# Kernel optimization log

Hardware: AMD Instinct MI355X
Metric: run time of the kernel (lower is better)

## Reference

```python
import jax, jax.numpy as jnp
import numpy as np
from jax import lax

BS, T, D, H, FF, KS, L = 8, 1024, 512, 8, 2048, 5, 6
DK = D // H  # 64


def setup_inputs() -> dict:
    key = jax.random.key(0)
    ks_ = jax.random.split(key, 16)
    n = lambda i, shape, s=0.02: jax.random.normal(ks_[i], shape, jnp.float32) * s
    return dict(
        q_embed_data=n(0, (BS, T, D), 1.0),
        qa_embed_data=n(1, (BS, T, D), 1.0),
        pid_embed_data=n(2, (BS, T, T), 1.0),  # unused for emb_type='qid'
        conv_w=n(3, (D, D, KS)), conv_b=jnp.zeros((D,), jnp.float32),
        sqrt_beta=n(4, (1, 1, D), 1.0),
        sm_g=jnp.ones((D,), jnp.float32), sm_b=jnp.zeros((D,), jnp.float32),
        k_w=n(5, (L, D, D)), k_b=jnp.zeros((L, D), jnp.float32),
        v_w=n(6, (L, D, D)), v_b=jnp.zeros((L, D), jnp.float32),
        out_w=n(7, (L, D, D)), out_b=jnp.zeros((L, D), jnp.float32),
        gammas=n(8, (L, H, 1, 1), 0.1),
        ln1_g=jnp.ones((L, D), jnp.float32), ln1_b=jnp.zeros((L, D), jnp.float32),
        ff1_w=n(9, (L, D, FF)), ff1_b=jnp.zeros((L, FF), jnp.float32),
        ff2_w=n(10, (L, FF, D)), ff2_b=jnp.zeros((L, D), jnp.float32),
        ln2_g=jnp.ones((L, D), jnp.float32), ln2_b=jnp.zeros((L, D), jnp.float32),
    )


def _layernorm(x, g, b, eps):
    m = jnp.mean(x, axis=-1, keepdims=True)
    v = jnp.mean((x - m) ** 2, axis=-1, keepdims=True)
    return g * (x - m) / jnp.sqrt(v + eps) + b


def _smooth(x, conv_w, conv_b, sqrt_beta, g, b):
    # x: [B,T,D]. Causal Conv1d: left-pad KS-1, crop to length T.
    xt = jnp.transpose(x, (0, 2, 1))  # [B,D,T]
    trend = lax.conv_general_dilated(
        xt, conv_w, window_strides=(1,), padding=[(KS - 1, 0)],
        dimension_numbers=('NCH', 'OIH', 'NCH')) + conv_b[None, :, None]
    trend = jnp.transpose(trend, (0, 2, 1))  # [B,T,D]
    random = x - trend
    seq = trend + sqrt_beta ** 2 * random
    return _layernorm(seq + x, g, b, 1e-12)


def _decay_attention(q, k, v, mask, gamma_param, zero_pad):
    # q,k,v: [B,H,T,DK]; mask: [1,1,T,T] bool
    neg = jnp.float32(-1e32)
    scores = jnp.einsum('bhqd,bhkd->bhqk', q, k) / np.float32(np.sqrt(DK))
    # detached distance-effect computation (no_grad in torch)
    s_ = jax.nn.softmax(jnp.where(mask, scores, neg), axis=-1) * mask.astype(jnp.float32)
    distcum = jnp.cumsum(s_, axis=-1)
    disttot = jnp.sum(s_, axis=-1, keepdims=True)
    idx = jnp.arange(T, dtype=jnp.float32)
    pos = jnp.abs(idx[None, :] - idx[:, None])[None, None]  # |j - i|
    dist = jnp.sqrt(jnp.clip((disttot - distcum) * pos, 0.0, None))
    dist = lax.stop_gradient(dist)
    gamma = -jax.nn.softplus(gamma_param)[None]  # [1,H,1,1]
    total_effect = jnp.clip(jnp.exp(dist * gamma), 1e-5, 1e5)
    scores = jnp.where(mask, scores * total_effect, neg)
    scores = jax.nn.softmax(scores, axis=-1)
    if zero_pad:
        scores = scores.at[:, :, 0, :].set(0.0)
    return jnp.einsum('bhqk,bhkd->bhqd', scores, v)


def _tlayer(p, i, mtype, q_in, k_in, v_in, apply_pos, masks):
    mask = masks[mtype]
    def heads(x, W, b):
        return jnp.transpose((x @ W + b).reshape(BS, T, H, DK), (0, 2, 1, 3))
    # kq_same=True: q and k both use k_linear
    q = heads(q_in, p['k_w'][i], p['k_b'][i])
    k = heads(k_in, p['k_w'][i], p['k_b'][i])
    v = heads(v_in, p['v_w'][i], p['v_b'][i])
    out = _decay_attention(q, k, v, mask, p['gammas'][i], zero_pad=(mtype == 0))
    concat = jnp.transpose(out, (0, 2, 1, 3)).reshape(BS, T, D)
    q2 = concat @ p['out_w'][i] + p['out_b'][i]
    x = _layernorm(q_in + q2, p['ln1_g'][i], p['ln1_b'][i], 1e-5)
    if apply_pos:
        hdn = jax.nn.relu(x @ p['ff1_w'][i] + p['ff1_b'][i])
        x = _layernorm(x + hdn @ p['ff2_w'][i] + p['ff2_b'][i],
                       p['ln2_g'][i], p['ln2_b'][i], 1e-5)
    return x


def _forward(q_embed_data, qa_embed_data, pid_embed_data,
             conv_w, conv_b, sqrt_beta, sm_g, sm_b,
             k_w, k_b, v_w, v_b, out_w, out_b, gammas,
             ln1_g, ln1_b, ff1_w, ff1_b, ff2_w, ff2_b, ln2_g, ln2_b):
    p = dict(k_w=k_w, k_b=k_b, v_w=v_w, v_b=v_b, out_w=out_w, out_b=out_b,
             gammas=gammas, ln1_g=ln1_g, ln1_b=ln1_b, ff1_w=ff1_w, ff1_b=ff1_b,
             ff2_w=ff2_w, ff2_b=ff2_b, ln2_g=ln2_g, ln2_b=ln2_b)
    tri = jnp.tril(jnp.ones((T, T), bool))
    masks = {1: tri[None, None], 0: jnp.tril(jnp.ones((T, T), bool), -1)[None, None]}
    x = _smooth(q_embed_data, conv_w, conv_b, sqrt_beta, sm_g, sm_b)
    y = _smooth(qa_embed_data, conv_w, conv_b, sqrt_beta, sm_g, sm_b)
    # blocks_1: n_blocks=2 layers, mask=1, self-attn on y
    y = _tlayer(p, 0, 1, y, y, y, True, masks)
    y = _tlayer(p, 1, 1, y, y, y, True, masks)
    # blocks_2: 4 layers alternating (mask=1, no FFN) / (mask=0, values=y, FFN)
    x = _tlayer(p, 2, 1, x, x, x, False, masks)
    x = _tlayer(p, 3, 0, x, x, y, True, masks)
    x = _tlayer(p, 4, 1, x, x, x, False, masks)
    x = _tlayer(p, 5, 0, x, x, y, True, masks)
    return x


def reference(q_embed_data, qa_embed_data, pid_embed_data,
              conv_w, conv_b, sqrt_beta, sm_g, sm_b,
              k_w, k_b, v_w, v_b, out_w, out_b, gammas,
              ln1_g, ln1_b, ff1_w, ff1_b, ff2_w, ff2_b, ln2_g, ln2_b):
    return _forward(q_embed_data, qa_embed_data, pid_embed_data,
                    conv_w, conv_b, sqrt_beta, sm_g, sm_b,
                    k_w, k_b, v_w, v_b, out_w, out_b, gammas,
                    ln1_g, ln1_b, ff1_w, ff1_b, ff2_w, ff2_b, ln2_g, ln2_b)
```

## Files before the change

### kernel.cpp

```cpp
#include <hip/hip_runtime.h>
#include <math.h>

#define T_  1024
#define D_  512
#define H_  8
#define DK_ 64
#define FF_ 2048
#define BSZ 8
#define M_  (BSZ * T_)
#define TP_ (T_ + 4)

typedef unsigned short u16;
typedef unsigned int u32;
typedef __attribute__((ext_vector_type(8))) __bf16 bf16x8;
typedef __attribute__((ext_vector_type(4))) float f32x4;

__device__ __forceinline__ u16 f2bf(float f) {
    unsigned int u = __float_as_uint(f);
    u += 0x7fffu + ((u >> 16) & 1u);
    return (u16)(u >> 16);
}
__device__ __forceinline__ float bf2f(u16 b) {
    return __uint_as_float((unsigned int)b << 16);
}

__device__ __forceinline__ void gload16(const void* g, void* l) {
    __builtin_amdgcn_global_load_lds(
        (const __attribute__((address_space(1))) void*)g,
        (__attribute__((address_space(3))) void*)l, 16, 0, 0);
}

__global__ void __launch_bounds__(256) gemm_mfma(
    const u16* __restrict__ A, const u16* __restrict__ Bt,
    const float* __restrict__ bias, void* __restrict__ Cout,
    int N, int K, int mode)
{
    __shared__ __align__(16) u16 As[128 * 32];
    __shared__ __align__(16) u16 Bs[128 * 32];
    int tid = threadIdx.x;
    int wid = tid >> 6, lane = tid & 63;
    int quad = lane >> 4, mrow = lane & 15;
    int m0 = blockIdx.y * 128, n0 = blockIdx.x * 128;
    int wr = (wid >> 1) * 64, wc = (wid & 1) * 64;

    const u16* Ap = A + (size_t)(m0 + (tid >> 2)) * K + (tid & 3) * 8;
    const u16* Bp = Bt + (size_t)(n0 + (tid >> 2)) * K + (tid & 3) * 8;
    char* lA = (char*)As + wid * 1024;
    char* lB = (char*)Bs + wid * 1024;

    f32x4 acc[4][4] = {};
    for (int k0 = 0; k0 < K; k0 += 32) {
        __syncthreads();
        gload16(Ap + k0, lA);
        gload16(Ap + (size_t)64 * K + k0, lA + 4096);
        gload16(Bp + k0, lB);
        gload16(Bp + (size_t)64 * K + k0, lB + 4096);
        asm volatile("s_waitcnt vmcnt(0)" ::: "memory");
        __syncthreads();
        bf16x8 af[4], bf[4];
#pragma unroll
        for (int t = 0; t < 4; ++t) {
            af[t] = *(const bf16x8*)&As[(wr + t * 16 + mrow) * 32 + quad * 8];
            bf[t] = *(const bf16x8*)&Bs[(wc + t * 16 + mrow) * 32 + quad * 8];
        }
#pragma unroll
        for (int rt = 0; rt < 4; ++rt)
#pragma unroll
            for (int ct = 0; ct < 4; ++ct)
                acc[rt][ct] = __builtin_amdgcn_mfma_f32_16x16x32_bf16(
                    af[rt], bf[ct], acc[rt][ct], 0, 0, 0);
    }

#pragma unroll
    for (int ct = 0; ct < 4; ++ct) {
        int col = n0 + wc + ct * 16 + mrow;
        float bv = bias ? bias[col] : 0.f;
#pragma unroll
        for (int rt = 0; rt < 4; ++rt) {
            int rowb = m0 + wr + rt * 16 + quad * 4;
            if (mode == 0) {
                float* C = (float*)Cout;
#pragma unroll
                for (int e = 0; e < 4; ++e)
                    C[(size_t)(rowb + e) * N + col] = acc[rt][ct][e] + bv;
            } else if (mode == 1) {
                u16* C = (u16*)Cout;
#pragma unroll
                for (int e = 0; e < 4; ++e)
                    C[(size_t)(rowb + e) * N + col] = f2bf(fmaxf(acc[rt][ct][e] + bv, 0.f));
            } else {
                u16* C = (u16*)Cout;
#pragma unroll
                for (int e = 0; e < 4; ++e)
                    C[(size_t)(rowb + e) * N + col] = f2bf(acc[rt][ct][e] + bv);
            }
        }
    }
}

__global__ void __launch_bounds__(256) gemm64_mfma(
    const u16* __restrict__ A, const u16* __restrict__ Bt,
    const float* __restrict__ bias, void* __restrict__ Cout,
    int N, int K, int mode)
{
    __shared__ __align__(16) u16 As[2 * 64 * 32];
    __shared__ __align__(16) u16 Bs[2 * 64 * 32];
    int tid = threadIdx.x;
    int wid = tid >> 6, lane = tid & 63;
    int quad = lane >> 4, mrow = lane & 15;
    int m0 = blockIdx.y * 64, n0 = blockIdx.x * 64;
    int wc = wid * 16;

    const u16* Ap = A + (size_t)(m0 + (tid >> 2)) * K + (tid & 3) * 8;
    const u16* Bp = Bt + (size_t)(n0 + (tid >> 2)) * K + (tid & 3) * 8;
    char* lA = (char*)As + wid * 1024;
    char* lB = (char*)Bs + wid * 1024;

    f32x4 acc[4] = {};
    for (int k0 = 0; k0 < K; k0 += 64) {
        __syncthreads();
        gload16(Ap + k0, lA);
        gload16(Ap + k0 + 32, lA + 4096);
        gload16(Bp + k0, lB);
        gload16(Bp + k0 + 32, lB + 4096);
        asm volatile("s_waitcnt vmcnt(0)" ::: "memory");
        __syncthreads();
#pragma unroll
        for (int q = 0; q < 2; ++q) {
            bf16x8 af[4];
#pragma unroll
            for (int t = 0; t < 4; ++t)
                af[t] = *(const bf16x8*)&As[q * 2048 + (t * 16 + mrow) * 32 + quad * 8];
            bf16x8 bf = *(const bf16x8*)&Bs[q * 2048 + (wc + mrow) * 32 + quad * 8];
#pragma unroll
            for (int rt = 0; rt < 4; ++rt)
                acc[rt] = __builtin_amdgcn_mfma_f32_16x16x32_bf16(af[rt], bf, acc[rt], 0, 0, 0);
        }
    }

    int col = n0 + wc + mrow;
    float bv = bias ? bias[col] : 0.f;
#pragma unroll
    for (int rt = 0; rt < 4; ++rt) {
        int rowb = m0 + rt * 16 + quad * 4;
        if (mode == 0) {
            float* C = (float*)Cout;
#pragma unroll
            for (int e = 0; e < 4; ++e)
                C[(size_t)(rowb + e) * N + col] = acc[rt][e] + bv;
        } else if (mode == 1) {
            u16* C = (u16*)Cout;
#pragma unroll
            for (int e = 0; e < 4; ++e)
                C[(size_t)(rowb + e) * N + col] = f2bf(fmaxf(acc[rt][e] + bv, 0.f));
        } else if (mode == 2) {
            u16* C = (u16*)Cout;
#pragma unroll
            for (int e = 0; e < 4; ++e)
                C[(size_t)(rowb + e) * N + col] = f2bf(acc[rt][e] + bv);
        } else {
            u16* C = (u16*)Cout;
            int h = col >> 6, dl = col & 63;
#pragma unroll
            for (int e = 0; e < 4; ++e) {
                int row = rowb + e;
                int b = row >> 10, t = row & (T_ - 1);
                C[(((size_t)(b * H_ + h) * DK_ + dl) << 10) + t] =
                    f2bf(acc[rt][e] + bv);
            }
        }
    }
}

__global__ void __launch_bounds__(256) conv64_mfma(
    const u16* __restrict__ Xp, const u16* __restrict__ W5t, float* __restrict__ C)
{
    __shared__ __align__(16) u16 As[2 * 64 * 32];
    __shared__ __align__(16) u16 Bs[2 * 64 * 32];
    int tid = threadIdx.x;
    int wid = tid >> 6, lane = tid & 63;
    int quad = lane >> 4, mrow = lane & 15;
    int m0 = blockIdx.y * 64, n0 = blockIdx.x * 64;
    int wc = wid * 16;
    int b = m0 >> 10, tloc = m0 & (T_ - 1);

    const u16* Ap0 = Xp + (size_t)(b * TP_ + tloc + (tid >> 2)) * D_ + (tid & 3) * 8;
    const u16* Bp0 = W5t + (size_t)(n0 + (tid >> 2)) * D_ + (tid & 3) * 8;
    char* lA = (char*)As + wid * 1024;
    char* lB = (char*)Bs + wid * 1024;

    f32x4 acc[4] = {};
    for (int s = 0; s < 40; ++s) {
        int ks = s >> 3, k0 = (s & 7) * 64;
        const u16* Ap = Ap0 + ks * D_ + k0;
        const u16* Bp = Bp0 + (size_t)ks * D_ * D_ + k0;
        __syncthreads();
        gload16(Ap, lA);
        gload16(Ap + 32, lA + 4096);
        gload16(Bp, lB);
        gload16(Bp + 32, lB + 4096);
        asm volatile("s_waitcnt vmcnt(0)" ::: "memory");
        __syncthreads();
#pragma unroll
        for (int q = 0; q < 2; ++q) {
            bf16x8 af[4];
#pragma unroll
            for (int t = 0; t < 4; ++t)
                af[t] = *(const bf16x8*)&As[q * 2048 + (t * 16 + mrow) * 32 + quad * 8];
            bf16x8 bf = *(const bf16x8*)&Bs[q * 2048 + (wc + mrow) * 32 + quad * 8];
#pragma unroll
            for (int rt = 0; rt < 4; ++rt)
                acc[rt] = __builtin_amdgcn_mfma_f32_16x16x32_bf16(af[rt], bf, acc[rt], 0, 0, 0);
        }
    }
    int col = n0 + wc + mrow;
#pragma unroll
    for (int rt = 0; rt < 4; ++rt) {
        int row = m0 + rt * 16 + quad * 4;
#pragma unroll
        for (int e = 0; e < 4; ++e)
            C[(size_t)(row + e) * D_ + col] = acc[rt][e];
    }
}

__global__ void __launch_bounds__(256) qk_mfma(
    const u16* __restrict__ Qh, u16* __restrict__ S)
{
    int kt = blockIdx.x, it = blockIdx.y;
    if (kt > it) return;
    int z = blockIdx.z;
    int b = z >> 3, h = z & 7;
    __shared__ __align__(16) u16 As[2 * 64 * 32];
    __shared__ __align__(16) u16 Bs[2 * 64 * 32];
    int tid = threadIdx.x;
    int wid = tid >> 6, lane = tid & 63;
    int quad = lane >> 4, mrow = lane & 15;
    int wc = wid * 16;

    const u16* Ap = Qh + (size_t)(b * T_ + it * 64 + (tid >> 2)) * D_ + h * DK_ + (tid & 3) * 8;
    const u16* Bp = Qh + (size_t)(b * T_ + kt * 64 + (tid >> 2)) * D_ + h * DK_ + (tid & 3) * 8;
    char* lA = (char*)As + wid * 1024;
    char* lB = (char*)Bs + wid * 1024;

    gload16(Ap, lA);
    gload16(Ap + 32, lA + 4096);
    gload16(Bp, lB);
    gload16(Bp + 32, lB + 4096);
    asm volatile("s_waitcnt vmcnt(0)" ::: "memory");
    __syncthreads();

    f32x4 acc[4] = {};
#pragma unroll
    for (int q = 0; q < 2; ++q) {
        bf16x8 af[4];
#pragma unroll
        for (int t = 0; t < 4; ++t)
            af[t] = *(const bf16x8*)&As[q * 2048 + (t * 16 + mrow) * 32 + quad * 8];
        bf16x8 bf = *(const bf16x8*)&Bs[q * 2048 + (wc + mrow) * 32 + quad * 8];
#pragma unroll
        for (int rt = 0; rt < 4; ++rt)
            acc[rt] = __builtin_amdgcn_mfma_f32_16x16x32_bf16(af[rt], bf, acc[rt], 0, 0, 0);
    }
    int col = kt * 64 + wc + mrow;
#pragma unroll
    for (int rt = 0; rt < 4; ++rt) {
        int row = it * 64 + rt * 16 + quad * 4;
#pragma unroll
        for (int e = 0; e < 4; ++e)
            S[((size_t)z * T_ + row + e) * T_ + col] = f2bf(acc[rt][e] * 0.125f);
    }
}

#define LOG2E 1.4426950408889634f

#define DPPF(OLDB, X, CTRL, RM) \
    __uint_as_float((u32)__builtin_amdgcn_update_dpp( \
        (int)(OLDB), __float_as_int(X), CTRL, RM, 0xf, false))

__device__ __forceinline__ float scan_add_f(float x) {
    x += DPPF(0u, x, 0x111, 0xf);
    x += DPPF(0u, x, 0x112, 0xf);
    x += DPPF(0u, x, 0x114, 0xf);
    x += DPPF(0u, x, 0x118, 0xf);
    x += DPPF(0u, x, 0x142, 0xa);
    x += DPPF(0u, x, 0x143, 0xc);
    return x;
}
__device__ __forceinline__ float scan_max_f(float x) {
    x = fmaxf(x, DPPF(0xff800000u, x, 0x111, 0xf));
    x = fmaxf(x, DPPF(0xff800000u, x, 0x112, 0xf));
    x = fmaxf(x, DPPF(0xff800000u, x, 0x114, 0xf));
    x = fmaxf(x, DPPF(0xff800000u, x, 0x118, 0xf));
    x = fmaxf(x, DPPF(0xff800000u, x, 0x142, 0xa));
    x = fmaxf(x, DPPF(0xff800000u, x, 0x143, 0xc));
    return x;
}
__device__ __forceinline__ float lane63(float x) {
    return __uint_as_float((u32)__builtin_amdgcn_readlane(__float_as_int(x), 63));
}

template<int NC>
__device__ __forceinline__ void decay_body(
    u16* __restrict__ row, int kmax, float gam, float fi, int lane, int wend)
{
    int base = lane * 2;
    float s0[NC], s1[NC], p0[NC], p1[NC];

    float mx = -1e30f;
#pragma unroll
    for (int c = 0; c < NC; ++c) {
        int k = c * 128 + base;
        u32 v = *(const u32*)(row + k);
        float a = __uint_as_float(v << 16) * LOG2E;
        float b = __uint_as_float(v & 0xffff0000u) * LOG2E;
        if (c == NC - 1) {
            a = (k     <= kmax) ? a : -1.5e30f;
            b = (k + 1 <= kmax) ? b : -1.5e30f;
        }
        s0[c] = a; s1[c] = b;
        mx = fmaxf(mx, fmaxf(a, b));
    }
    mx = lane63(scan_max_f(mx));

    float t1 = 0.f;
#pragma unroll
    for (int c = 0; c < NC; ++c) {
        float e0 = __builtin_amdgcn_exp2f(s0[c] - mx);
        float e1 = __builtin_amdgcn_exp2f(s1[c] - mx);
        p0[c] = e0; p1[c] = e1;
        t1 += e0 + e1;
    }
    float tot = lane63(scan_add_f(t1));
    float inv1 = __builtin_amdgcn_rcpf(tot);
    float mx2 = fmaxf(mx, 0.f);

    float t2 = 0.f;
    float running = 0.f;
    float kf = (float)base;
#pragma unroll
    for (int c = 0; c < NC; ++c) {
        float sc = scan_add_f(p0[c] + p1[c]);
        float incl1 = running + sc;
        float incl0 = incl1 - p1[c];
        running += lane63(sc);
        float rem0 = fmaxf((tot - incl0) * inv1, 0.f);
        float rem1 = fmaxf((tot - incl1) * inv1, 0.f);
        float pos0 = fabsf(kf - fi);
        float pos1 = fabsf(kf + 1.f - fi);
        float ef0 = __builtin_amdgcn_fmed3f(
            __builtin_amdgcn_exp2f(sqrtf(rem0 * pos0) * gam), 1e-5f, 1e5f);
        float ef1 = __builtin_amdgcn_fmed3f(
            __builtin_amdgcn_exp2f(sqrtf(rem1 * pos1) * gam), 1e-5f, 1e5f);
        float e0 = __builtin_amdgcn_exp2f(s0[c] * ef0 - mx2);
        float e1 = __builtin_amdgcn_exp2f(s1[c] * ef1 - mx2);
        p0[c] = e0; p1[c] = e1;
        t2 += e0 + e1;
        kf += 128.f;
    }
    float inv2 = __builtin_amdgcn_rcpf(lane63(scan_add_f(t2)));

#pragma unroll
    for (int c = 0; c < NC; ++c) {
        float lo = p0[c] * inv2, hi = p1[c] * inv2;
        u32 o;
        asm("v_cvt_pk_bf16_f32 %0, %1, %2" : "=v"(o) : "v"(lo), "v"(hi));
        *(u32*)(row + c * 128 + base) = o;
    }
    for (int c = NC; c < wend; ++c)
        *(u32*)(row + c * 128 + base) = 0u;
}

__global__ void __launch_bounds__(256) decay_rows(
    u16* __restrict__ S, const float* __restrict__ gam_l, int mtype)
{
    int tid = threadIdx.x;
    int wv = tid >> 6, lane = tid & 63;
    int i = blockIdx.x * 4 + wv;
    int z = blockIdx.y;
    int h = z & 7;
    u16* row = S + ((size_t)z * T_ + i) * T_;
    int kmax = (mtype == 0) ? (i - 1) : i;

    if (kmax < 0) {
        row[lane] = 0;
        return;
    }
    int nc   = (kmax >> 7) + 1;
    int wend = (((i >> 6) + 1) * 64 + 127) >> 7;
    float gam = -log1pf(__expf(gam_l[h])) * LOG2E;
    float fi = (float)i;

    switch (nc) {
        case 1: decay_body<1>(row, kmax, gam, fi, lane, wend); break;
        case 2: decay_body<2>(row, kmax, gam, fi, lane, wend); break;
        case 3: decay_body<3>(row, kmax, gam, fi, lane, wend); break;
        case 4: decay_body<4>(row, kmax, gam, fi, lane, wend); break;
        case 5: decay_body<5>(row, kmax, gam, fi, lane, wend); break;
        case 6: decay_body<6>(row, kmax, gam, fi, lane, wend); break;
        case 7: decay_body<7>(row, kmax, gam, fi, lane, wend); break;
        default: decay_body<8>(row, kmax, gam, fi, lane, wend); break;
    }
}

__global__ void __launch_bounds__(256) pv_mfma(
    const u16* __restrict__ P, const u16* __restrict__ Vt,
    u16* __restrict__ O)
{
    int mt = blockIdx.x;
    int z = blockIdx.y;
    int b = z >> 3, h = z & 7;
    __shared__ __align__(16) u16 As[2 * 64 * 32];
    __shared__ __align__(16) u16 Bs[2 * 64 * 32];
    int tid = threadIdx.x;
    int wid = tid >> 6, lane = tid & 63;
    int quad = lane >> 4, mrow = lane & 15;
    int wc = wid * 16;

    const u16* Ap = P + ((size_t)z * T_ + mt * 64 + (tid >> 2)) * T_ + (tid & 3) * 8;
    const u16* Bp = Vt + ((size_t)z * DK_ + (tid >> 2)) * T_ + (tid & 3) * 8;
    char* lA = (char*)As + wid * 1024;
    char* lB = (char*)Bs + wid * 1024;

    int kend = (mt + 1) * 64;
    f32x4 acc[4] = {};
    for (int k0 = 0; k0 < kend; k0 += 64) {
        __syncthreads();
        gload16(Ap + k0, lA);
        gload16(Ap + k0 + 32, lA + 4096);
        gload16(Bp + k0, lB);
        gload16(Bp + k0 + 32, lB + 4096);
        asm volatile("s_waitcnt vmcnt(0)" ::: "memory");
        __syncthreads();
#pragma unroll
        for (int q = 0; q < 2; ++q) {
            bf16x8 af[4];
#pragma unroll
            for (int t = 0; t < 4; ++t)
                af[t] = *(const bf16x8*)&As[q * 2048 + (t * 16 + mrow) * 32 + quad * 8];
            bf16x8 bf = *(const bf16x8*)&Bs[q * 2048 + (wc + mrow) * 32 + quad * 8];
#pragma unroll
            for (int rt = 0; rt < 4; ++rt)
                acc[rt] = __builtin_amdgcn_mfma_f32_16x16x32_bf16(af[rt], bf, acc[rt], 0, 0, 0);
        }
    }
    int col = h * DK_ + wc + mrow;
#pragma unroll
    for (int rt = 0; rt < 4; ++rt) {
        int row = b * T_ + mt * 64 + rt * 16 + quad * 4;
#pragma unroll
        for (int e = 0; e < 4; ++e)
            O[(size_t)(row + e) * D_ + col] = f2bf(acc[rt][e]);
    }
}

__global__ void __launch_bounds__(256) transpose_bf16(
    const float* __restrict__ W, u16* __restrict__ Wt, int K, int N)
{
    __shared__ float tile[32][33];
    size_t base = (size_t)blockIdx.z * K * N;
    W += base; Wt += base;
    int k0 = blockIdx.y * 32, n0 = blockIdx.x * 32;
    int r = threadIdx.x >> 3, c = (threadIdx.x & 7) * 4;
    float4 v = *(const float4*)(W + (size_t)(k0 + r) * N + n0 + c);
    tile[r][c] = v.x; tile[r][c + 1] = v.y; tile[r][c + 2] = v.z; tile[r][c + 3] = v.w;
    __syncthreads();
    ushort4 o;
    o.x = f2bf(tile[c + 0][r]); o.y = f2bf(tile[c + 1][r]);
    o.z = f2bf(tile[c + 2][r]); o.w = f2bf(tile[c + 3][r]);
    *(ushort4*)(Wt + (size_t)(n0 + r) * K + k0 + c) = o;
}

__global__ void w5_gather(const float* __restrict__ cw, u16* __restrict__ W5t)
{
    int idx = blockIdx.x * 256 + threadIdx.x;
    if (idx >= 5 * D_ * D_) return;
    int ks = idx / (D_ * D_);
    int rem = idx - ks * (D_ * D_);
    int o = rem >> 9, i = rem & (D_ - 1);
    W5t[idx] = f2bf(cw[((size_t)o * D_ + i) * 5 + ks]);
}

__global__ void cast_pad(const float* __restrict__ x, const float* __restrict__ y,
                         u16* __restrict__ Xp, u16* __restrict__ Yp)
{
    int idx = blockIdx.x * 256 + threadIdx.x;
    if (idx >= BSZ * TP_ * D_) return;
    int d = idx & (D_ - 1);
    int rowp = idx >> 9;
    int b = rowp / TP_;
    int t = rowp - b * TP_;
    u16 vx = 0, vy = 0;
    if (t >= 4) {
        size_t src = ((size_t)(b * T_ + t - 4) << 9) + d;
        vx = f2bf(x[src]); vy = f2bf(y[src]);
    }
    Xp[idx] = vx; Yp[idx] = vy;
}

__global__ void __launch_bounds__(256) smooth_ln(
    const float* __restrict__ x, const float* __restrict__ trend,
    const float* __restrict__ conv_b, const float* __restrict__ sqrt_beta,
    const float* __restrict__ g, const float* __restrict__ bb,
    float* __restrict__ out, u16* __restrict__ outb)
{
    __shared__ float s_red[8];
    int row = blockIdx.x, tid = threadIdx.x;
    int lane = tid & 63, wid = tid >> 6;
    float2 xv = ((const float2*)(x + (size_t)row * D_))[tid];
    float2 tv = ((const float2*)(trend + (size_t)row * D_))[tid];
    float2 cb = ((const float2*)conv_b)[tid];
    float2 sb = ((const float2*)sqrt_beta)[tid];
    float t0 = tv.x + cb.x, t1 = tv.y + cb.y;
    float v0 = t0 + sb.x * sb.x * (xv.x - t0) + xv.x;
    float v1 = t1 + sb.y * sb.y * (xv.y - t1) + xv.y;
    float s = v0 + v1, sq = v0 * v0 + v1 * v1;
    for (int o = 32; o > 0; o >>= 1) { s += __shfl_xor(s, o, 64); sq += __shfl_xor(sq, o, 64); }
    if (lane == 0) { s_red[wid] = s; s_red[4 + wid] = sq; }
    __syncthreads();
    s = s_red[0] + s_red[1] + s_red[2] + s_red[3];
    sq = s_red[4] + s_red[5] + s_red[6] + s_red[7];
    float mean = s * (1.f / D_);
    float var = sq * (1.f / D_) - mean * mean;
    if (var < 0.f) var = 0.f;
    float rstd = rsqrtf(var + 1e-12f);
    float2 gv = ((const float2*)g)[tid];
    float2 bv = ((const float2*)bb)[tid];
    float2 o2;
    o2.x = gv.x * (v0 - mean) * rstd + bv.x;
    o2.y = gv.y * (v1 - mean) * rstd + bv.y;
    ((float2*)(out + (size_t)row * D_))[tid] = o2;
    ushort2 ob; ob.x = f2bf(o2.x); ob.y = f2bf(o2.y);
    ((ushort2*)(outb + (size_t)row * D_))[tid] = ob;
}

__global__ void __launch_bounds__(256) add_ln(
    const float* __restrict__ a, const float* __restrict__ c,
    const float* __restrict__ g, const float* __restrict__ bb,
    float* __restrict__ out, u16* __restrict__ outb, float eps)
{
    __shared__ float s_red[8];
    int row = blockIdx.x, tid = threadIdx.x;
    int lane = tid & 63, wid = tid >> 6;
    float2 av = ((const float2*)(a + (size_t)row * D_))[tid];
    float2 cv = ((const float2*)(c + (size_t)row * D_))[tid];
    float v0 = av.x + cv.x;
    float v1 = av.y + cv.y;
    float s = v0 + v1, sq = v0 * v0 + v1 * v1;
    for (int o = 32; o > 0; o >>= 1) { s += __shfl_xor(s, o, 64); sq += __shfl_xor(sq, o, 64); }
    if (lane == 0) { s_red[wid] = s; s_red[4 + wid] = sq; }
    __syncthreads();
    s = s_red[0] + s_red[1] + s_red[2] + s_red[3];
    sq = s_red[4] + s_red[5] + s_red[6] + s_red[7];
    float mean = s * (1.f / D_);
    float var = sq * (1.f / D_) - mean * mean;
    if (var < 0.f) var = 0.f;
    float rstd = rsqrtf(var + eps);
    float2 gv = ((const float2*)g)[tid];
    float2 bv = ((const float2*)bb)[tid];
    float2 o2;
    o2.x = gv.x * (v0 - mean) * rstd + bv.x;
    o2.y = gv.y * (v1 - mean) * rstd + bv.y;
    ((float2*)(out + (size_t)row * D_))[tid] = o2;
    ushort2 ob; ob.x = f2bf(o2.x); ob.y = f2bf(o2.y);
    ((ushort2*)(outb + (size_t)row * D_))[tid] = ob;
}

extern "C" void kernel_launch(void* const* d_in, const int* in_sizes, int n_in,
                              void* d_out, int out_size, void* d_ws, size_t ws_size,
                              hipStream_t stream)
{
    const float* q_embed   = (const float*)d_in[0];
    const float* qa_embed  = (const float*)d_in[1];
    const float* conv_w    = (const float*)d_in[3];
    const float* conv_b    = (const float*)d_in[4];
    const float* sqrt_beta = (const float*)d_in[5];
    const float* sm_g      = (const float*)d_in[6];
    const float* sm_b      = (const float*)d_in[7];
    const float* k_w       = (const float*)d_in[8];
    const float* k_b       = (const float*)d_in[9];
    const float* v_w       = (const float*)d_in[10];
    const float* v_b       = (const float*)d_in[11];
    const float* out_w     = (const float*)d_in[12];
    const float* out_b     = (const float*)d_in[13];
    const float* gammas    = (const float*)d_in[14];
    const float* ln1_g     = (const float*)d_in[15];
    const float* ln1_b     = (const float*)d_in[16];
    const float* ff1_w     = (const float*)d_in[17];
    const float* ff1_b     = (const float*)d_in[18];
    const float* ff2_w     = (const float*)d_in[19];
    const float* ff2_b     = (const float*)d_in[20];
    const float* ln2_g     = (const float*)d_in[21];
    const float* ln2_b     = (const float*)d_in[22];

    const size_t NT = (size_t)M_ * D_;
    float* X = (float*)d_out;
    char* w = (char*)d_ws;
    float* Y  = (float*)w; w += NT * 4;
    float* Fb = (float*)w; w += NT * 4;
    u16* Sb = (u16*)w;
    u16* Hb = Sb;
    u16* Xpad = Sb;
    u16* Ypad = Xpad + (size_t)BSZ * TP_ * D_;
    u16* W5t  = Ypad + (size_t)BSZ * TP_ * D_;
    w += (size_t)BSZ * H_ * T_ * T_ * 2;
    u16* Xb  = (u16*)w; w += NT * 2;
    u16* Yb  = (u16*)w; w += NT * 2;
    u16* Cb  = (u16*)w; w += NT * 2;
    u16* Qh  = (u16*)w; w += NT * 2;
    u16* Vt  = (u16*)w; w += NT * 2;
    u16* KWt = (u16*)w; w += (size_t)6 * D_ * D_ * 2;
    u16* VWt = (u16*)w; w += (size_t)6 * D_ * D_ * 2;
    u16* OWt = (u16*)w; w += (size_t)6 * D_ * D_ * 2;
    u16* F1t = (u16*)w; w += (size_t)6 * D_ * FF_ * 2;
    u16* F2t = (u16*)w; w += (size_t)6 * FF_ * D_ * 2;

    dim3 blk(256);

    cast_pad<<<(BSZ * TP_ * D_ + 255) / 256, blk, 0, stream>>>(q_embed, qa_embed, Xpad, Ypad);
    w5_gather<<<(5 * D_ * D_ + 255) / 256, blk, 0, stream>>>(conv_w, W5t);
    transpose_bf16<<<dim3(D_ / 32, D_ / 32, 6), blk, 0, stream>>>(k_w, KWt, D_, D_);
    transpose_bf16<<<dim3(D_ / 32, D_ / 32, 6), blk, 0, stream>>>(v_w, VWt, D_, D_);
    transpose_bf16<<<dim3(D_ / 32, D_ / 32, 6), blk, 0, stream>>>(out_w, OWt, D_, D_);
    transpose_bf16<<<dim3(FF_ / 32, D_ / 32, 6), blk, 0, stream>>>(ff1_w, F1t, D_, FF_);
    transpose_bf16<<<dim3(D_ / 32, FF_ / 32, 6), blk, 0, stream>>>(ff2_w, F2t, FF_, D_);

    conv64_mfma<<<dim3(8, 128), blk, 0, stream>>>(Xpad, W5t, Fb);
    smooth_ln<<<M_, blk, 0, stream>>>(q_embed, Fb, conv_b, sqrt_beta, sm_g, sm_b, X, Xb);
    conv64_mfma<<<dim3(8, 128), blk, 0, stream>>>(Ypad, W5t, Fb);
    smooth_ln<<<M_, blk, 0, stream>>>(qa_embed, Fb, conv_b, sqrt_beta, sm_g, sm_b, Y, Yb);

    auto layer = [&](int l, int mtype, float* io, u16* iob, const u16* vinb, bool ffn) {
        gemm64_mfma<<<dim3(8, 128), blk, 0, stream>>>(iob, KWt + (size_t)l * D_ * D_,
                                                      k_b + (size_t)l * D_, Qh, D_, D_, 2);
        gemm64_mfma<<<dim3(8, 128), blk, 0, stream>>>(vinb, VWt + (size_t)l * D_ * D_,
                                                      v_b + (size_t)l * D_, Vt, D_, D_, 3);
        qk_mfma<<<dim3(16, 16, 64), blk, 0, stream>>>(Qh, Sb);
        decay_rows<<<dim3(T_ / 4, 64), blk, 0, stream>>>(Sb, gammas + l * H_, mtype);
        pv_mfma<<<dim3(16, 64), blk, 0, stream>>>(Sb, Vt, Cb);
        gemm64_mfma<<<dim3(8, 128), blk, 0, stream>>>(Cb, OWt + (size_t)l * D_ * D_,
                                                      out_b + (size_t)l * D_, Fb, D_, D_, 0);
        add_ln<<<M_, blk, 0, stream>>>(io, Fb, ln1_g + l * D_, ln1_b + l * D_, io, iob, 1e-5f);
        if (ffn) {
            gemm_mfma<<<dim3(16, 64), blk, 0, stream>>>(iob, F1t + (size_t)l * D_ * FF_,
                                                        ff1_b + (size_t)l * FF_, Hb, FF_, D_, 1);
            gemm64_mfma<<<dim3(8, 128), blk, 0, stream>>>(Hb, F2t + (size_t)l * FF_ * D_,
                                                          ff2_b + (size_t)l * D_, Fb, D_, FF_, 0);
            add_ln<<<M_, blk, 0, stream>>>(io, Fb, ln2_g + l * D_, ln2_b + l * D_, io, iob, 1e-5f);
        }
    };

    layer(0, 1, Y, Yb, Yb, true);
    layer(1, 1, Y, Yb, Yb, true);
    layer(2, 1, X, Xb, Xb, false);
    layer(3, 0, X, Xb, Yb, true);
    layer(4, 1, X, Xb, Xb, false);
    layer(5, 0, X, Xb, Yb, true);
}
```

Baseline: 1.694 ms.

## Deepen GEMM K-steps per barrier and batch K/V, conv and smooth launches

The GEMM, conv and PV kernels now load 128-wide K slices per barrier instead of 64 (64 instead of 32 for the large GEMM), using larger LDS buffers. This halves the number of sync and wait-for-memory round trips per output tile. The separate K and V projection GEMMs are merged into one launch using blockIdx.z, and likewise the two conv and two smooth_ln passes. This cuts launch count and improves occupancy, at the cost of more LDS per block, which may lower concurrent blocks per CU. The second conv output buffer reuses the Qh/Vt scratch region.

```diff
diff --git a/kernel.cpp b/kernel.cpp
--- a/kernel.cpp
+++ b/kernel.cpp
@@ -35,8 +35,8 @@
     const float* __restrict__ bias, void* __restrict__ Cout,
     int N, int K, int mode)
 {
-    __shared__ __align__(16) u16 As[128 * 32];
-    __shared__ __align__(16) u16 Bs[128 * 32];
+    __shared__ __align__(16) u16 As[2 * 128 * 32];
+    __shared__ __align__(16) u16 Bs[2 * 128 * 32];
     int tid = threadIdx.x;
     int wid = tid >> 6, lane = tid & 63;
     int quad = lane >> 4, mrow = lane & 15;
@@ -49,26 +49,33 @@
     char* lB = (char*)Bs + wid * 1024;
 
     f32x4 acc[4][4] = {};
-    for (int k0 = 0; k0 < K; k0 += 32) {
+    for (int k0 = 0; k0 < K; k0 += 64) {
         __syncthreads();
         gload16(Ap + k0, lA);
         gload16(Ap + (size_t)64 * K + k0, lA + 4096);
+        gload16(Ap + k0 + 32, lA + 8192);
+        gload16(Ap + (size_t)64 * K + k0 + 32, lA + 8192 + 4096);
         gload16(Bp + k0, lB);
         gload16(Bp + (size_t)64 * K + k0, lB + 4096);
+        gload16(Bp + k0 + 32, lB + 8192);
+        gload16(Bp + (size_t)64 * K + k0 + 32, lB + 8192 + 4096);
         asm volatile("s_waitcnt vmcnt(0)" ::: "memory");
         __syncthreads();
-        bf16x8 af[4], bf[4];
-#pragma unroll
-        for (int t = 0; t < 4; ++t) {
-            af[t] = *(const bf16x8*)&As[(wr + t * 16 + mrow) * 32 + quad * 8];
-            bf[t] = *(const bf16x8*)&Bs[(wc + t * 16 + mrow) * 32 + quad * 8];
+#pragma unroll
+        for (int q = 0; q < 2; ++q) {
+            bf16x8 af[4], bf[4];
+#pragma unroll
+            for (int t = 0; t < 4; ++t) {
+                af[t] = *(const bf16x8*)&As[q * 4096 + (wr + t * 16 + mrow) * 32 + quad * 8];
+                bf[t] = *(const bf16x8*)&Bs[q * 4096 + (wc + t * 16 + mrow) * 32 + quad * 8];
+            }
+#pragma unroll
+            for (int rt = 0; rt < 4; ++rt)
+#pragma unroll
+                for (int ct = 0; ct < 4; ++ct)
+                    acc[rt][ct] = __builtin_amdgcn_mfma_f32_16x16x32_bf16(
+                        af[rt], bf[ct], acc[rt][ct], 0, 0, 0);
         }
-#pragma unroll
-        for (int rt = 0; rt < 4; ++rt)
-#pragma unroll
-            for (int ct = 0; ct < 4; ++ct)
-                acc[rt][ct] = __builtin_amdgcn_mfma_f32_16x16x32_bf16(
-                    af[rt], bf[ct], acc[rt][ct], 0, 0, 0);
     }
 
 #pragma unroll
@@ -98,47 +105,38 @@
     }
 }
 
-__global__ void __launch_bounds__(256) gemm64_mfma(
-    const u16* __restrict__ A, const u16* __restrict__ Bt,
-    const float* __restrict__ bias, void* __restrict__ Cout,
-    int N, int K, int mode)
-{
-    __shared__ __align__(16) u16 As[2 * 64 * 32];
-    __shared__ __align__(16) u16 Bs[2 * 64 * 32];
-    int tid = threadIdx.x;
-    int wid = tid >> 6, lane = tid & 63;
-    int quad = lane >> 4, mrow = lane & 15;
-    int m0 = blockIdx.y * 64, n0 = blockIdx.x * 64;
-    int wc = wid * 16;
-
-    const u16* Ap = A + (size_t)(m0 + (tid >> 2)) * K + (tid & 3) * 8;
-    const u16* Bp = Bt + (size_t)(n0 + (tid >> 2)) * K + (tid & 3) * 8;
-    char* lA = (char*)As + wid * 1024;
-    char* lB = (char*)Bs + wid * 1024;
-
-    f32x4 acc[4] = {};
-    for (int k0 = 0; k0 < K; k0 += 64) {
-        __syncthreads();
-        gload16(Ap + k0, lA);
-        gload16(Ap + k0 + 32, lA + 4096);
-        gload16(Bp + k0, lB);
-        gload16(Bp + k0 + 32, lB + 4096);
-        asm volatile("s_waitcnt vmcnt(0)" ::: "memory");
-        __syncthreads();
-#pragma unroll
-        for (int q = 0; q < 2; ++q) {
-            bf16x8 af[4];
-#pragma unroll
-            for (int t = 0; t < 4; ++t)
-                af[t] = *(const bf16x8*)&As[q * 2048 + (t * 16 + mrow) * 32 + quad * 8];
-            bf16x8 bf = *(const bf16x8*)&Bs[q * 2048 + (wc + mrow) * 32 + quad * 8];
-#pragma unroll
-            for (int rt = 0; rt < 4; ++rt)
-                acc[rt] = __builtin_amdgcn_mfma_f32_16x16x32_bf16(af[rt], bf, acc[rt], 0, 0, 0);
-        }
-    }
-
-    int col = n0 + wc + mrow;
+__device__ __forceinline__ void g64_step128(
+    const u16* Ap, const u16* Bp, char* lA, char* lB,
+    const u16* As, const u16* Bs, int mrow, int quad, int wc, f32x4 acc[4])
+{
+    __syncthreads();
+    gload16(Ap, lA);
+    gload16(Ap + 32, lA + 4096);
+    gload16(Ap + 64, lA + 8192);
+    gload16(Ap + 96, lA + 12288);
+    gload16(Bp, lB);
+    gload16(Bp + 32, lB + 4096);
+    gload16(Bp + 64, lB + 8192);
+    gload16(Bp + 96, lB + 12288);
+    asm volatile("s_waitcnt vmcnt(0)" ::: "memory");
+    __syncthreads();
+#pragma unroll
+    for (int q = 0; q < 4; ++q) {
+        bf16x8 af[4];
+#pragma unroll
+        for (int t = 0; t < 4; ++t)
+            af[t] = *(const bf16x8*)&As[q * 2048 + (t * 16 + mrow) * 32 + quad * 8];
+        bf16x8 bf = *(const bf16x8*)&Bs[q * 2048 + (wc + mrow) * 32 + quad * 8];
+#pragma unroll
+        for (int rt = 0; rt < 4; ++rt)
+            acc[rt] = __builtin_amdgcn_mfma_f32_16x16x32_bf16(af[rt], bf, acc[rt], 0, 0, 0);
+    }
+}
+
+__device__ __forceinline__ void g64_epilogue(
+    f32x4 acc[4], const float* bias, void* Cout, int N, int mode,
+    int m0, int col, int quad, int mrow)
+{
     float bv = bias ? bias[col] : 0.f;
 #pragma unroll
     for (int rt = 0; rt < 4; ++rt) {
@@ -172,11 +170,75 @@
     }
 }
 
+__global__ void __launch_bounds__(256) gemm64_mfma(
+    const u16* __restrict__ A, const u16* __restrict__ Bt,
+    const float* __restrict__ bias, void* __restrict__ Cout,
+    int N, int K, int mode)
+{
+    __shared__ __align__(16) u16 As[4 * 64 * 32];
+    __shared__ __align__(16) u16 Bs[4 * 64 * 32];
+    int tid = threadIdx.x;
+    int wid = tid >> 6, lane = tid & 63;
+    int quad = lane >> 4, mrow = lane & 15;
+    int m0 = blockIdx.y * 64, n0 = blockIdx.x * 64;
+    int wc = wid * 16;
+
+    const u16* Ap = A + (size_t)(m0 + (tid >> 2)) * K + (tid & 3) * 8;
+    const u16* Bp = Bt + (size_t)(n0 + (tid >> 2)) * K + (tid & 3) * 8;
+    char* lA = (char*)As + wid * 1024;
+    char* lB = (char*)Bs + wid * 1024;
+
+    f32x4 acc[4] = {};
+    for (int k0 = 0; k0 < K; k0 += 128)
+        g64_step128(Ap + k0, Bp + k0, lA, lB, As, Bs, mrow, quad, wc, acc);
+
+    g64_epilogue(acc, bias, Cout, N, mode, m0, n0 + wc + mrow, quad, mrow);
+}
+
+__global__ void __launch_bounds__(256) gemm64_kv(
+    const u16* __restrict__ A1, const u16* __restrict__ B1,
+    const float* __restrict__ b1, void* __restrict__ O1,
+    const u16* __restrict__ A2, const u16* __restrict__ B2,
+    const float* __restrict__ b2, void* __restrict__ O2)
+{
+    __shared__ __align__(16) u16 As[4 * 64 * 32];
+    __shared__ __align__(16) u16 Bs[4 * 64 * 32];
+    int z = blockIdx.z;
+    const u16* A = z ? A2 : A1;
+    const u16* Bt = z ? B2 : B1;
+    const float* bias = z ? b2 : b1;
+    void* Cout = z ? O2 : O1;
+    int mode = z ? 3 : 2;
+
+    int tid = threadIdx.x;
+    int wid = tid >> 6, lane = tid & 63;
+    int quad = lane >> 4, mrow = lane & 15;
+    int m0 = blockIdx.y * 64, n0 = blockIdx.x * 64;
+    int wc = wid * 16;
+
+    const u16* Ap = A + (size_t)(m0 + (tid >> 2)) * D_ + (tid & 3) * 8;
+    const u16* Bp = Bt + (size_t)(n0 + (tid >> 2)) * D_ + (tid & 3) * 8;
+    char* lA = (char*)As + wid * 1024;
+    char* lB = (char*)Bs + wid * 1024;
+
+    f32x4 acc[4] = {};
+    for (int k0 = 0; k0 < D_; k0 += 128)
+        g64_step128(Ap + k0, Bp + k0, lA, lB, As, Bs, mrow, quad, wc, acc);
+
+    g64_epilogue(acc, bias, Cout, D_, mode, m0, n0 + wc + mrow, quad, mrow);
+}
+
 __global__ void __launch_bounds__(256) conv64_mfma(
-    const u16* __restrict__ Xp, const u16* __restrict__ W5t, float* __restrict__ C)
-{
-    __shared__ __align__(16) u16 As[2 * 64 * 32];
-    __shared__ __align__(16) u16 Bs[2 * 64 * 32];
+    const u16* __restrict__ Xp, const u16* __restrict__ Yp,
+    const u16* __restrict__ W5t,
+    float* __restrict__ Cx, float* __restrict__ Cy)
+{
+    __shared__ __align__(16) u16 As[4 * 64 * 32];
+    __shared__ __align__(16) u16 Bs[4 * 64 * 32];
+    int z = blockIdx.z;
+    const u16* Xin = z ? Yp : Xp;
+    float* C = z ? Cy : Cx;
+
     int tid = threadIdx.x;
     int wid = tid >> 6, lane = tid & 63;
     int quad = lane >> 4, mrow = lane & 15;
@@ -184,34 +246,16 @@
     int wc = wid * 16;
     int b = m0 >> 10, tloc = m0 & (T_ - 1);
 
-    const u16* Ap0 = Xp + (size_t)(b * TP_ + tloc + (tid >> 2)) * D_ + (tid & 3) * 8;
+    const u16* Ap0 = Xin + (size_t)(b * TP_ + tloc + (tid >> 2)) * D_ + (tid & 3) * 8;
     const u16* Bp0 = W5t + (size_t)(n0 + (tid >> 2)) * D_ + (tid & 3) * 8;
     char* lA = (char*)As + wid * 1024;
     char* lB = (char*)Bs + wid * 1024;
 
     f32x4 acc[4] = {};
-    for (int s = 0; s < 40; ++s) {
-        int ks = s >> 3, k0 = (s & 7) * 64;
-        const u16* Ap = Ap0 + ks * D_ + k0;
-        const u16* Bp = Bp0 + (size_t)ks * D_ * D_ + k0;
-        __syncthreads();
-        gload16(Ap, lA);
-        gload16(Ap + 32, lA + 4096);
-        gload16(Bp, lB);
-        gload16(Bp + 32, lB + 4096);
-        asm volatile("s_waitcnt vmcnt(0)" ::: "memory");
-        __syncthreads();
-#pragma unroll
-        for (int q = 0; q < 2; ++q) {
-            bf16x8 af[4];
-#pragma unroll
-            for (int t = 0; t < 4; ++t)
-                af[t] = *(const bf16x8*)&As[q * 2048 + (t * 16 + mrow) * 32 + quad * 8];
-            bf16x8 bf = *(const bf16x8*)&Bs[q * 2048 + (wc + mrow) * 32 + quad * 8];
-#pragma unroll
-            for (int rt = 0; rt < 4; ++rt)
-                acc[rt] = __builtin_amdgcn_mfma_f32_16x16x32_bf16(af[rt], bf, acc[rt], 0, 0, 0);
-        }
+    for (int s = 0; s < 20; ++s) {
+        int ks = s >> 2, k0 = (s & 3) * 128;
+        g64_step128(Ap0 + ks * D_ + k0, Bp0 + (size_t)ks * D_ * D_ + k0,
+                    lA, lB, As, Bs, mrow, quad, wc, acc);
     }
     int col = n0 + wc + mrow;
 #pragma unroll
@@ -409,8 +453,8 @@
     int mt = blockIdx.x;
     int z = blockIdx.y;
     int b = z >> 3, h = z & 7;
-    __shared__ __align__(16) u16 As[2 * 64 * 32];
-    __shared__ __align__(16) u16 Bs[2 * 64 * 32];
+    __shared__ __align__(16) u16 As[4 * 64 * 32];
+    __shared__ __align__(16) u16 Bs[4 * 64 * 32];
     int tid = threadIdx.x;
     int wid = tid >> 6, lane = tid & 63;
     int quad = lane >> 4, mrow = lane & 15;
@@ -423,7 +467,10 @@
 
     int kend = (mt + 1) * 64;
     f32x4 acc[4] = {};
-    for (int k0 = 0; k0 < kend; k0 += 64) {
+    int k0 = 0;
+    for (; k0 + 128 <= kend; k0 += 128)
+        g64_step128(Ap + k0, Bp + k0, lA, lB, As, Bs, mrow, quad, wc, acc);
+    if (k0 < kend) {
         __syncthreads();
         gload16(Ap + k0, lA);
         gload16(Ap + k0 + 32, lA + 4096);
@@ -498,13 +545,20 @@
 }
 
 __global__ void __launch_bounds__(256) smooth_ln(
-    const float* __restrict__ x, const float* __restrict__ trend,
+    const float* __restrict__ x1, const float* __restrict__ x2,
+    const float* __restrict__ tr1, const float* __restrict__ tr2,
     const float* __restrict__ conv_b, const float* __restrict__ sqrt_beta,
     const float* __restrict__ g, const float* __restrict__ bb,
-    float* __restrict__ out, u16* __restrict__ outb)
+    float* __restrict__ out1, u16* __restrict__ outb1,
+    float* __restrict__ out2, u16* __restrict__ outb2)
 {
     __shared__ float s_red[8];
     int row = blockIdx.x, tid = threadIdx.x;
+    int zz = blockIdx.y;
+    const float* x = zz ? x2 : x1;
+    const float* trend = zz ? tr2 : tr1;
+    float* out = zz ? out2 : out1;
+    u16* outb = zz ? outb2 : outb1;
     int lane = tid & 63, wid = tid >> 6;
     float2 xv = ((const float2*)(x + (size_t)row * D_))[tid];
     float2 tv = ((const float2*)(trend + (size_t)row * D_))[tid];
@@ -613,6 +667,7 @@
     u16* OWt = (u16*)w; w += (size_t)6 * D_ * D_ * 2;
     u16* F1t = (u16*)w; w += (size_t)6 * D_ * FF_ * 2;
     u16* F2t = (u16*)w; w += (size_t)6 * FF_ * D_ * 2;
+    float* Fb2 = (float*)Qh;
 
     dim3 blk(256);
 
@@ -624,16 +679,15 @@
     transpose_bf16<<<dim3(FF_ / 32, D_ / 32, 6), blk, 0, stream>>>(ff1_w, F1t, D_, FF_);
     transpose_bf16<<<dim3(D_ / 32, FF_ / 32, 6), blk, 0, stream>>>(ff2_w, F2t, FF_, D_);
 
-    conv64_mfma<<<dim3(8, 128), blk, 0, stream>>>(Xpad, W5t, Fb);
-    smooth_ln<<<M_, blk, 0, stream>>>(q_embed, Fb, conv_b, sqrt_beta, sm_g, sm_b, X, Xb);
-    conv64_mfma<<<dim3(8, 128), blk, 0, stream>>>(Ypad, W5t, Fb);
-    smooth_ln<<<M_, blk, 0, stream>>>(qa_embed, Fb, conv_b, sqrt_beta, sm_g, sm_b, Y, Yb);
+    conv64_mfma<<<dim3(8, 128, 2), blk, 0, stream>>>(Xpad, Ypad, W5t, Fb, Fb2);
+    smooth_ln<<<dim3(M_, 2), blk, 0, stream>>>(q_embed, qa_embed, Fb, Fb2,
+                                               conv_b, sqrt_beta, sm_g, sm_b,
+                                               X, Xb, Y, Yb);
 
     auto layer = [&](int l, int mtype, float* io, u16* iob, const u16* vinb, bool ffn) {
-        gemm64_mfma<<<dim3(8, 128), blk, 0, stream>>>(iob, KWt + (size_t)l * D_ * D_,
-                                                      k_b + (size_t)l * D_, Qh, D_, D_, 2);
-        gemm64_mfma<<<dim3(8, 128), blk, 0, stream>>>(vinb, VWt + (size_t)l * D_ * D_,
-                                                      v_b + (size_t)l * D_, Vt, D_, D_, 3);
+        gemm64_kv<<<dim3(8, 128, 2), blk, 0, stream>>>(
+            iob, KWt + (size_t)l * D_ * D_, k_b + (size_t)l * D_, Qh,
+            vinb, VWt + (size_t)l * D_ * D_, v_b + (size_t)l * D_, Vt);
         qk_mfma<<<dim3(16, 16, 64), blk, 0, stream>>>(Qh, Sb);
         decay_rows<<<dim3(T_ / 4, 64), blk, 0, stream>>>(Sb, gammas + l * H_, mtype);
         pv_mfma<<<dim3(16, 64), blk, 0, stream>>>(Sb, Vt, Cb);
```

New measurement: 1.706 ms. Within noise of the previous version (+0.7%).
